# Optimization experiments

Hardware: AMD Instinct MI355X
Metric: run time of the kernel (lower is better)

## Reference

```python
import jax, jax.numpy as jnp
import numpy as np

B, T, IN, H = 16, 1024, 1024, 1024


def setup_inputs() -> dict:
    key = jax.random.key(0)
    ks = jax.random.split(key, 6)
    s_in = 1.0 / np.sqrt(IN)
    s_out = 1.0 / np.sqrt(2 * H)
    return {
        "x": jax.random.normal(ks[0], (B, T, IN), jnp.float32),
        "W_in": jax.random.uniform(ks[1], (H, IN), jnp.float32, -s_in, s_in),
        "b_in": jax.random.uniform(ks[2], (H,), jnp.float32, -s_in, s_in),
        "leak_tau_v": jax.random.normal(ks[3], (H,), jnp.float32),
        "flip_threshold": jnp.full((H,), 0.5, jnp.float32),
        "W_out": jax.random.uniform(ks[4], (H, 2 * H), jnp.float32, -s_out, s_out),
        "b_out": jax.random.uniform(ks[5], (H,), jnp.float32, -s_out, s_out),
    }


def _hsru_scan(I_tbh, alpha, thr):
    """Leaky-integrate / threshold-reset recurrence over time.
    I_tbh: [T,B,H]; alpha, thr: [H]. Returns (v_seq, spike_seq) each [T,B,H].
    v_t = alpha*v_{t-1} + I_t; spike on crossing threshold; v reset on spike.
    """
    def step(v, I_t):
        v = alpha * v + I_t
        spike = (v > thr).astype(v.dtype)  # hard threshold; zero grad (as in torch)
        v = v * (1.0 - spike)              # reset membrane on flip
        return v, (v, spike)

    v0 = jnp.zeros(I_tbh.shape[1:], I_tbh.dtype)
    _, (v_seq, s_seq) = jax.lax.scan(step, v0, I_tbh)
    return v_seq, s_seq


def reference(x, W_in, b_in, leak_tau_v, flip_threshold, W_out, b_out):
    # input currents: [B,T,H]
    I = jnp.einsum('bti,hi->bth', x, W_in) + b_in
    alpha = jnp.exp(-jax.nn.softplus(leak_tau_v))  # [H], in (0,1)
    v_seq, s_seq = _hsru_scan(jnp.swapaxes(I, 0, 1), alpha, flip_threshold)
    combined = jnp.concatenate([v_seq, s_seq], axis=-1)   # [T,B,2H]
    combined = jnp.swapaxes(combined, 0, 1)               # [B,T,2H]
    return jnp.tanh(jnp.einsum('btk,hk->bth', combined, W_out) + b_out)
```

## Files before the change

kernel.cpp:

```cpp
#include <hip/hip_runtime.h>
#include <hip/hip_bf16.h>
#include <cmath>


typedef __attribute__((ext_vector_type(8))) __bf16 bf16x8;
typedef __attribute__((ext_vector_type(4))) __bf16 bf16x4;
typedef __attribute__((ext_vector_type(4))) float  f32x4;

#define LDT 40
#define LDF 36

__global__ __launch_bounds__(256)
void gemm1_f32chain_kernel(const float* __restrict__ X,
                           const float* __restrict__ W,
                           const float* __restrict__ bias,
                           float* __restrict__ I)
{
    __shared__ __align__(16) float sA[128][LDF];
    __shared__ __align__(16) float sB[128][LDF];

    const int tid  = threadIdx.x;
    const int bn   = blockIdx.x;
    const int bm   = blockIdx.y;
    const int row0 = bm * 128;
    const int col0 = bn * 128;
    const int tx   = tid & 15;
    const int ty   = tid >> 4;

    int rr[4], cc[4];
    #pragma unroll
    for (int i = 0; i < 4; ++i) {
        int q = tid + i * 256;
        rr[i] = q >> 3;
        cc[i] = (q & 7) * 4;
    }

    f32x4 av[4], bv[4];

    float acc[8][8];
    #pragma unroll
    for (int i = 0; i < 8; ++i)
        #pragma unroll
        for (int j = 0; j < 8; ++j)
            acc[i][j] = 0.0f;

    #pragma unroll
    for (int i = 0; i < 4; ++i) {
        av[i] = *(const f32x4*)&X[(size_t)(row0 + rr[i]) * 1024 + cc[i]];
        bv[i] = *(const f32x4*)&W[(size_t)(col0 + rr[i]) * 1024 + cc[i]];
    }

    for (int k0 = 0; k0 < 1024; k0 += 32) {
        __syncthreads();
        #pragma unroll
        for (int i = 0; i < 4; ++i) {
            *(f32x4*)&sA[rr[i]][cc[i]] = av[i];
            *(f32x4*)&sB[rr[i]][cc[i]] = bv[i];
        }
        __syncthreads();

        if (k0 + 32 < 1024) {
            const int kn = k0 + 32;
            #pragma unroll
            for (int i = 0; i < 4; ++i) {
                av[i] = *(const f32x4*)&X[(size_t)(row0 + rr[i]) * 1024 + kn + cc[i]];
                bv[i] = *(const f32x4*)&W[(size_t)(col0 + rr[i]) * 1024 + kn + cc[i]];
            }
        }

        #pragma unroll
        for (int kk = 0; kk < 32; kk += 4) {
            f32x4 a4[8], b4[8];
            #pragma unroll
            for (int i = 0; i < 8; ++i) a4[i] = *(const f32x4*)&sA[ty + 16 * i][kk];
            #pragma unroll
            for (int j = 0; j < 8; ++j) b4[j] = *(const f32x4*)&sB[tx + 16 * j][kk];
            #pragma unroll
            for (int q = 0; q < 4; ++q)
                #pragma unroll
                for (int i = 0; i < 8; ++i)
                    #pragma unroll
                    for (int j = 0; j < 8; ++j)
                        acc[i][j] = fmaf(a4[i][q], b4[j][q], acc[i][j]);
        }
    }

    #pragma unroll
    for (int i = 0; i < 8; ++i)
        #pragma unroll
        for (int j = 0; j < 8; ++j) {
            int rg = row0 + ty + 16 * i;
            int cg = col0 + tx + 16 * j;
            I[(size_t)rg * 1024 + cg] = __fadd_rn(acc[i][j], bias[cg]);
        }
}

__global__ void hsru_scan_f32_kernel(const float* __restrict__ I,
                                     const float* __restrict__ leak,
                                     const float* __restrict__ thr,
                                     __bf16* __restrict__ comb)
{
    int g = blockIdx.x * blockDim.x + threadIdx.x;
    int b = g >> 10;
    int h = g & 1023;

    float lt = leak[h];
    float e     = (float)exp(-(double)fabsf(lt));
    float l1    = (float)log1p((double)e);
    float sp    = __fadd_rn(fmaxf(lt, 0.0f), l1);
    float alpha = (float)exp(-(double)sp);
    float th    = thr[h];

    const float* Ip = I    + (size_t)b * (1024 * 1024) + h;
    __bf16*      cp = comb + (size_t)b * (1024 * 2048) + h;

    float v = 0.0f;
    #pragma unroll 4
    for (int t = 0; t < 1024; ++t) {
        float cur = Ip[(size_t)t * 1024];
        v = __fadd_rn(__fmul_rn(alpha, v), cur);
        float spike = (v > th) ? 1.0f : 0.0f;
        v = __fmul_rn(v, __fsub_rn(1.0f, spike));
        cp[(size_t)t * 2048]        = (__bf16)v;
        cp[(size_t)t * 2048 + 1024] = (__bf16)spike;
    }
}

__global__ __launch_bounds__(256)
void wcvt_kernel(const float* __restrict__ W, __bf16* __restrict__ Wb)
{
    int idx = (blockIdx.x * 256 + threadIdx.x) * 8;
    f32x4 v0 = *(const f32x4*)&W[idx];
    f32x4 v1 = *(const f32x4*)&W[idx + 4];
    bf16x8 o;
    #pragma unroll
    for (int j = 0; j < 4; ++j) { o[j] = (__bf16)v0[j]; o[4 + j] = (__bf16)v1[j]; }
    *(bf16x8*)&Wb[idx] = o;
}

__global__ __launch_bounds__(256)
void gemm2_kernel(const __bf16* __restrict__ A,
                  const __bf16* __restrict__ Wb,
                  const float* __restrict__ bias,
                  float* __restrict__ O)
{
    __shared__ __align__(16) __bf16 sA[128][LDT];
    __shared__ __align__(16) __bf16 sB[128][LDT];

    const int tid  = threadIdx.x;
    const int bn   = blockIdx.x;
    const int bm   = blockIdx.y;
    const int row0 = bm * 128;
    const int col0 = bn * 128;

    const int lane = tid & 63;
    const int wid  = tid >> 6;
    const int wm   = (wid >> 1) * 64;
    const int wn   = (wid & 1) * 64;

    f32x4 acc[4][4];
    #pragma unroll
    for (int i = 0; i < 4; ++i)
        #pragma unroll
        for (int j = 0; j < 4; ++j)
            acc[i][j] = f32x4{0.f, 0.f, 0.f, 0.f};

    const int frow  = lane & 15;
    const int fkoff = (lane >> 4) * 8;

    for (int k0 = 0; k0 < 2048; k0 += 32) {
        #pragma unroll
        for (int i = 0; i < 2; ++i) {
            int q  = tid + i * 256;
            int r  = q >> 2;
            int c8 = (q & 3) * 8;
            *(bf16x8*)&sA[r][c8] = *(const bf16x8*)&A [(size_t)(row0 + r) * 2048 + k0 + c8];
            *(bf16x8*)&sB[r][c8] = *(const bf16x8*)&Wb[(size_t)(col0 + r) * 2048 + k0 + c8];
        }
        __syncthreads();

        bf16x8 a_f[4], b_f[4];
        #pragma unroll
        for (int f = 0; f < 4; ++f) {
            a_f[f] = *(const bf16x8*)&sA[wm + f * 16 + frow][fkoff];
            b_f[f] = *(const bf16x8*)&sB[wn + f * 16 + frow][fkoff];
        }
        #pragma unroll
        for (int fm = 0; fm < 4; ++fm)
            #pragma unroll
            for (int fn = 0; fn < 4; ++fn)
                acc[fm][fn] = __builtin_amdgcn_mfma_f32_16x16x32_bf16(a_f[fm], b_f[fn], acc[fm][fn], 0, 0, 0);
        __syncthreads();
    }

    const int crow = (lane >> 4) * 4;
    const int ccol = lane & 15;
    #pragma unroll
    for (int fm = 0; fm < 4; ++fm)
        #pragma unroll
        for (int fn = 0; fn < 4; ++fn)
            #pragma unroll
            for (int j = 0; j < 4; ++j) {
                int rg = row0 + wm + fm * 16 + crow + j;
                int cg = col0 + wn + fn * 16 + ccol;
                O[(size_t)rg * 1024 + cg] = tanhf(acc[fm][fn][j] + bias[cg]);
            }
}

extern "C" void kernel_launch(void* const* d_in, const int* in_sizes, int n_in,
                              void* d_out, int out_size, void* d_ws, size_t ws_size,
                              hipStream_t stream)
{
    const float* x     = (const float*)d_in[0];
    const float* W_in  = (const float*)d_in[1];
    const float* b_in  = (const float*)d_in[2];
    const float* leak  = (const float*)d_in[3];
    const float* thr   = (const float*)d_in[4];
    const float* W_out = (const float*)d_in[5];
    const float* b_out = (const float*)d_in[6];

    const size_t NEED = (64ull << 20) + (4ull << 20);
    if (ws_size < NEED) return;

    float*  out  = (float*)d_out;
    __bf16* comb = (__bf16*)d_ws;
    __bf16* Wb   = (__bf16*)((char*)d_ws + (64ull << 20));

    dim3 grid(8, 128);

    wcvt_kernel<<<1024, 256, 0, stream>>>(W_out, Wb);
    gemm1_f32chain_kernel<<<grid, 256, 0, stream>>>(x, W_in, b_in, out);
    hsru_scan_f32_kernel<<<64, 256, 0, stream>>>(out, leak, thr, comb);
    gemm2_kernel<<<grid, 256, 0, stream>>>(comb, Wb, b_out, out);
}
```

Baseline: 663.0 us.

## Double-buffer GEMM1 shared tiles and prefetch scan inputs in register blocks

GEMM1 moves from register-staged prefetch to two shared-memory buffers, each loaded straight from global, with one barrier per k-step instead of two. The scan kernel now loads 16 timesteps of input ahead into registers, hiding the latency of its serial dependent loads. It also launches as 256 blocks of 64 threads so the 16384 independent chains spread across more compute units. The GEMM1 change removes the overlap of global loads with compute and may expose more load latency, and doubles shared memory use.

```diff
diff --git a/kernel.cpp b/kernel.cpp
--- a/kernel.cpp
+++ b/kernel.cpp
@@ -16,8 +16,8 @@
                            const float* __restrict__ bias,
                            float* __restrict__ I)
 {
-    __shared__ __align__(16) float sA[128][LDF];
-    __shared__ __align__(16) float sB[128][LDF];
+    __shared__ __align__(16) float sA[2][128][LDF];
+    __shared__ __align__(16) float sB[2][128][LDF];
 
     const int tid  = threadIdx.x;
     const int bn   = blockIdx.x;
@@ -35,8 +35,6 @@
         cc[i] = (q & 7) * 4;
     }
 
-    f32x4 av[4], bv[4];
-
     float acc[8][8];
     #pragma unroll
     for (int i = 0; i < 8; ++i)
@@ -44,37 +42,26 @@
         for (int j = 0; j < 8; ++j)
             acc[i][j] = 0.0f;
 
-    #pragma unroll
-    for (int i = 0; i < 4; ++i) {
-        av[i] = *(const f32x4*)&X[(size_t)(row0 + rr[i]) * 1024 + cc[i]];
-        bv[i] = *(const f32x4*)&W[(size_t)(col0 + rr[i]) * 1024 + cc[i]];
-    }
-
-    for (int k0 = 0; k0 < 1024; k0 += 32) {
+    for (int t = 0; t < 32; ++t) {
+        const int p  = t & 1;
+        const int k0 = t * 32;
+
+        #pragma unroll
+        for (int i = 0; i < 4; ++i) {
+            f32x4 va = *(const f32x4*)&X[(size_t)(row0 + rr[i]) * 1024 + k0 + cc[i]];
+            f32x4 vb = *(const f32x4*)&W[(size_t)(col0 + rr[i]) * 1024 + k0 + cc[i]];
+            *(f32x4*)&sA[p][rr[i]][cc[i]] = va;
+            *(f32x4*)&sB[p][rr[i]][cc[i]] = vb;
+        }
         __syncthreads();
-        #pragma unroll
-        for (int i = 0; i < 4; ++i) {
-            *(f32x4*)&sA[rr[i]][cc[i]] = av[i];
-            *(f32x4*)&sB[rr[i]][cc[i]] = bv[i];
-        }
-        __syncthreads();
-
-        if (k0 + 32 < 1024) {
-            const int kn = k0 + 32;
-            #pragma unroll
-            for (int i = 0; i < 4; ++i) {
-                av[i] = *(const f32x4*)&X[(size_t)(row0 + rr[i]) * 1024 + kn + cc[i]];
-                bv[i] = *(const f32x4*)&W[(size_t)(col0 + rr[i]) * 1024 + kn + cc[i]];
-            }
-        }
 
         #pragma unroll
         for (int kk = 0; kk < 32; kk += 4) {
             f32x4 a4[8], b4[8];
             #pragma unroll
-            for (int i = 0; i < 8; ++i) a4[i] = *(const f32x4*)&sA[ty + 16 * i][kk];
-            #pragma unroll
-            for (int j = 0; j < 8; ++j) b4[j] = *(const f32x4*)&sB[tx + 16 * j][kk];
+            for (int i = 0; i < 8; ++i) a4[i] = *(const f32x4*)&sA[p][ty + 16 * i][kk];
+            #pragma unroll
+            for (int j = 0; j < 8; ++j) b4[j] = *(const f32x4*)&sB[p][tx + 16 * j][kk];
             #pragma unroll
             for (int q = 0; q < 4; ++q)
                 #pragma unroll
@@ -95,12 +82,13 @@
         }
 }
 
-__global__ void hsru_scan_f32_kernel(const float* __restrict__ I,
-                                     const float* __restrict__ leak,
-                                     const float* __restrict__ thr,
-                                     __bf16* __restrict__ comb)
-{
-    int g = blockIdx.x * blockDim.x + threadIdx.x;
+__global__ __launch_bounds__(64)
+void hsru_scan_f32_kernel(const float* __restrict__ I,
+                          const float* __restrict__ leak,
+                          const float* __restrict__ thr,
+                          __bf16* __restrict__ comb)
+{
+    int g = blockIdx.x * 64 + threadIdx.x;
     int b = g >> 10;
     int h = g & 1023;
 
@@ -114,15 +102,30 @@
     const float* Ip = I    + (size_t)b * (1024 * 1024) + h;
     __bf16*      cp = comb + (size_t)b * (1024 * 2048) + h;
 
+    float buf[16], nxt[16];
+    #pragma unroll
+    for (int j = 0; j < 16; ++j) buf[j] = Ip[(size_t)j * 1024];
+
     float v = 0.0f;
-    #pragma unroll 4
-    for (int t = 0; t < 1024; ++t) {
-        float cur = Ip[(size_t)t * 1024];
-        v = __fadd_rn(__fmul_rn(alpha, v), cur);
-        float spike = (v > th) ? 1.0f : 0.0f;
-        v = __fmul_rn(v, __fsub_rn(1.0f, spike));
-        cp[(size_t)t * 2048]        = (__bf16)v;
-        cp[(size_t)t * 2048 + 1024] = (__bf16)spike;
+    for (int t0 = 0; t0 < 1024; t0 += 16) {
+        if (t0 + 16 < 1024) {
+            #pragma unroll
+            for (int j = 0; j < 16; ++j)
+                nxt[j] = Ip[(size_t)(t0 + 16 + j) * 1024];
+        }
+        #pragma unroll
+        for (int j = 0; j < 16; ++j) {
+            float cur = buf[j];
+            v = __fadd_rn(__fmul_rn(alpha, v), cur);
+            float spike = (v > th) ? 1.0f : 0.0f;
+            v = __fmul_rn(v, __fsub_rn(1.0f, spike));
+            cp[(size_t)(t0 + j) * 2048]        = (__bf16)v;
+            cp[(size_t)(t0 + j) * 2048 + 1024] = (__bf16)spike;
+        }
+        if (t0 + 16 < 1024) {
+            #pragma unroll
+            for (int j = 0; j < 16; ++j) buf[j] = nxt[j];
+        }
     }
 }
 
@@ -230,6 +233,6 @@
 
     wcvt_kernel<<<1024, 256, 0, stream>>>(W_out, Wb);
     gemm1_f32chain_kernel<<<grid, 256, 0, stream>>>(x, W_in, b_in, out);
-    hsru_scan_f32_kernel<<<64, 256, 0, stream>>>(out, leak, thr, comb);
+    hsru_scan_f32_kernel<<<256, 64, 0, stream>>>(out, leak, thr, comb);
     gemm2_kernel<<<grid, 256, 0, stream>>>(comb, Wb, b_out, out);
 }
```

New measurement: 671.3 us. Within noise of the previous version (+1.2%).
